# Kernel optimization log

Measured on AMD Instinct MI355X. Metric: run time of the kernel, lower is better.

The kernel has to match this reference:

```python
import jax, jax.numpy as jnp
import numpy as np

K = 64        # num_clusters
S1 = 5        # num_shadow + 1
C = 128       # dim
ALPHA = 1500.0
EPS = 1e-12


def setup_inputs() -> dict:
    key = jax.random.key(0)
    k1, k2 = jax.random.split(key)
    x = jax.random.normal(k1, (8, C, 44, 44), dtype=jnp.float32)
    centroids = jax.random.normal(k2, (K, S1, C), dtype=jnp.float32) * 0.01
    return {"x": x, "centroids": centroids}


def reference(x, centroids):
    N = x.shape[0]
    # conv params derived from centroids, as in _init_params
    w = (2.0 * ALPHA) * centroids.reshape(K * S1, C)            # (K*S1, C)
    b = -ALPHA * jnp.linalg.norm(centroids.reshape(K * S1, C), axis=1)  # (K*S1,)

    xf = x.reshape(N, C, -1)                                    # (N, C, P)
    # 1x1 conv == GEMM over channel dim
    logits = jnp.einsum('mc,ncp->nmp', w, xf) + b[None, :, None]
    logits = logits.reshape(N, K, S1, -1)                       # (N, K, S1, P)

    soft_alpha = jax.nn.softmax(logits[:, :, 0:1, :], axis=1)   # (N, K, 1, P)
    soft_beta = jax.nn.softmax(logits, axis=2)[:, :, 0:1, :]    # (N, K, 1, P)
    soft_assign = soft_alpha * soft_beta                        # (N, K, 1, P)

    # residual = x - rep_centroid; then residual *= (1 + soft_assign); sum over P.
    # sum_p (x[n,c,p] - rep[k,c]) * w[n,k,p]
    #   = einsum(w, x) - rep[k,c] * sum_p w[n,k,p]   (same math, no (N,K,C,P) tensor)
    w_assign = 1.0 + soft_assign[:, :, 0, :]                    # (N, K, P)
    rep = centroids[:, 0, :]                                    # (K, C)
    out = jnp.einsum('nkp,ncp->nkc', w_assign, xf) \
          - rep[None, :, :] * jnp.sum(w_assign, axis=-1)[:, :, None]  # (N, K, C)

    # intra-cluster L2 normalize (dim=2), flatten, global L2 normalize
    out = out / jnp.maximum(jnp.linalg.norm(out, axis=2, keepdims=True), EPS)
    flat = out.reshape(N, -1)
    flat = flat / jnp.maximum(jnp.linalg.norm(flat, axis=1, keepdims=True), EPS)
    return (flat, soft_assign)
```

## Files before the change

### kernel.cpp

```cpp
#include <hip/hip_runtime.h>
#include <math.h>

#define NB 8
#define KC 64
#define S1C 5
#define CC 128
#define PP 1936
#define MM 320
#define PT 64
#define NPT 31
#define NTILE (NB * NPT)
#define ALPHAF 1500.0f
#define EPSF 1e-12f

#define WS_PS   ((size_t)NTILE * KC * CC)
#define WS_MAIN_FLOATS (WS_PS + (size_t)NTILE * KC)
#define WS_FB_ZERO_BYTES ((size_t)(NB * KC * CC + NB * KC) * 4)

typedef __attribute__((ext_vector_type(8))) short short8;
typedef __attribute__((ext_vector_type(4))) float f32x4;

__device__ __forceinline__ unsigned pack_bf16s(float x) {
    unsigned u  = __float_as_uint(x);
    unsigned hi = u & 0xffff0000u;
    float lo    = x - __uint_as_float(hi);
    return hi | (__float_as_uint(lo) >> 16);
}

__device__ __forceinline__ void unpack8(const int4 q0, const int4 q1,
                                        short8& h, short8& l) {
    const int d[8] = {q0.x, q0.y, q0.z, q0.w, q1.x, q1.y, q1.z, q1.w};
#pragma unroll
    for (int j = 0; j < 8; ++j) {
        h[j] = (short)((unsigned)d[j] >> 16);
        l[j] = (short)((unsigned)d[j] & 0xffffu);
    }
}

__device__ __forceinline__ void split8(const float4 a, const float4 b,
                                       short8& h, short8& l) {
    const float f[8] = {a.x, a.y, a.z, a.w, b.x, b.y, b.z, b.w};
#pragma unroll
    for (int j = 0; j < 8; ++j) {
        const unsigned u  = __float_as_uint(f[j]);
        const unsigned hi = u & 0xffff0000u;
        const float lo    = f[j] - __uint_as_float(hi);
        h[j] = (short)(hi >> 16);
        l[j] = (short)(__float_as_uint(lo) >> 16);
    }
}

__global__ __launch_bounds__(1024, 4) void k1_main(
    const float* __restrict__ x, const float* __restrict__ cen,
    float* __restrict__ sa_out, float* __restrict__ outC,
    float* __restrict__ outS, int mode)
{
    __shared__ unsigned xbuf[CC * 68];
    __shared__ unsigned war[KC * 68];
    __shared__ float2   ap[16 * 66];
    __shared__ float    bias_p[512];

    const int tid  = threadIdx.x;
    const int lane = tid & 63;
    const int wid  = tid >> 6;
    const int quad = lane >> 4;
    const int l15  = lane & 15;
    const int bx   = blockIdx.x;
    const int n    = bx / NPT;
    const int pt   = bx - n * NPT;
    const int p0   = pt * PT;

    const float* xn = x + (size_t)n * CC * PP;
    for (int idx = tid; idx < CC * 16; idx += 1024) {
        const int c = idx >> 4;
        const int q = idx & 15;
        const int p = 4 * q;
        float4 v = make_float4(0.f, 0.f, 0.f, 0.f);
        if (p0 + p < PP) v = *(const float4*)(xn + (size_t)c * PP + p0 + p);
        xbuf[(p + 0) * 132 + c] = pack_bf16s(v.x);
        xbuf[(p + 1) * 132 + c] = pack_bf16s(v.y);
        xbuf[(p + 2) * 132 + c] = pack_bf16s(v.z);
        xbuf[(p + 3) * 132 + c] = pack_bf16s(v.w);
    }
    if (tid < 192) bias_p[8 * (tid / 3) + 5 + (tid % 3)] = -3.0e38f;
    if (tid < MM) {
        const float4* row = (const float4*)(cen + (size_t)tid * CC);
        float ss = 0.f;
#pragma unroll
        for (int c4 = 0; c4 < 32; ++c4) {
            const float4 v = row[c4];
            ss += v.x * v.x + v.y * v.y + v.z * v.z + v.w * v.w;
        }
        bias_p[8 * (tid / 5) + (tid % 5)] = -ALPHAF * sqrtf(ss);
    }
    __syncthreads();

    f32x4 dacc[4][2];
#pragma unroll
    for (int a = 0; a < 4; ++a) {
        dacc[a][0] = (f32x4){0.f, 0.f, 0.f, 0.f};
        dacc[a][1] = (f32x4){0.f, 0.f, 0.f, 0.f};
    }
    int mp[2], wrow[2]; bool wvalid[2];
#pragma unroll
    for (int i = 0; i < 2; ++i) {
        mp[i] = (2 * wid + i) * 16 + l15;
        const int s = mp[i] & 7;
        wvalid[i] = (s < 5);
        wrow[i] = 5 * (mp[i] >> 3) + s;
    }

#pragma unroll 1
    for (int ks = 0; ks < 4; ++ks) {
        short8 bh[2], bl[2];
#pragma unroll
        for (int i = 0; i < 2; ++i) {
            float4 wlo = make_float4(0.f, 0.f, 0.f, 0.f);
            float4 whi = make_float4(0.f, 0.f, 0.f, 0.f);
            if (wvalid[i]) {
                const float* wp = cen + (size_t)wrow[i] * CC + ks * 32 + quad * 8;
                wlo = *(const float4*)wp;
                whi = *(const float4*)(wp + 4);
            }
            split8(wlo, whi, bh[i], bl[i]);
        }
#pragma unroll
        for (int a = 0; a < 4; ++a) {
            const int abase = (a * 16 + l15) * 132 + ks * 32 + quad * 8;
            const int4 q0 = *(const int4*)(&xbuf[abase]);
            const int4 q1 = *(const int4*)(&xbuf[abase + 4]);
            short8 ah, al;
            unpack8(q0, q1, ah, al);
#pragma unroll
            for (int i = 0; i < 2; ++i) {
                dacc[a][i] = __builtin_amdgcn_mfma_f32_16x16x32_bf16(ah, bh[i], dacc[a][i], 0, 0, 0);
                dacc[a][i] = __builtin_amdgcn_mfma_f32_16x16x32_bf16(ah, bl[i], dacc[a][i], 0, 0, 0);
                dacc[a][i] = __builtin_amdgcn_mfma_f32_16x16x32_bf16(al, bh[i], dacc[a][i], 0, 0, 0);
            }
        }
    }

    const float bv0 = bias_p[mp[0]];
    const float bv1 = bias_p[mp[1]];
#pragma unroll
    for (int a = 0; a < 4; ++a)
#pragma unroll
        for (int r = 0; r < 4; ++r) {
            dacc[a][0][r] = 2.f * ALPHAF * dacc[a][0][r] + bv0;
            dacc[a][1][r] = 2.f * ALPHAF * dacc[a][1][r] + bv1;
        }

#pragma unroll
    for (int a = 0; a < 4; ++a) {
        f32x4 mx4, se4;
#pragma unroll
        for (int r = 0; r < 4; ++r) {
            float m_ = fmaxf(dacc[a][0][r], dacc[a][1][r]);
            m_ = fmaxf(m_, __shfl_xor(m_, 8));
            float se = __expf(dacc[a][0][r] - m_) + __expf(dacc[a][1][r] - m_);
            se += __shfl_xor(se, 8);
            mx4[r] = m_; se4[r] = se;
        }
        if (l15 == 0) {
#pragma unroll
            for (int r = 0; r < 4; ++r)
                ap[wid * 66 + a * 16 + 4 * quad + r] = make_float2(mx4[r], se4[r]);
        }
    }
    __syncthreads();

    float gmv, arv;
    {
        float gm = -3.0e38f;
#pragma unroll
        for (int w = 0; w < 16; ++w) gm = fmaxf(gm, ap[w * 66 + lane].x);
        float s = 0.f;
#pragma unroll
        for (int w = 0; w < 16; ++w) {
            const float2 v = ap[w * 66 + lane];
            s += v.y * __expf(v.x - gm);
        }
        gmv = gm; arv = 1.0f / s;
    }

    float* san = sa_out + (size_t)n * KC * PP;
    float psum[2] = {0.f, 0.f};
    const bool is_s0 = ((l15 & 7) == 0);
#pragma unroll
    for (int a = 0; a < 4; ++a) {
#pragma unroll
        for (int i = 0; i < 2; ++i) {
            const f32x4 lg = dacc[a][i];
            f32x4 sav; unsigned wpk[4];
#pragma unroll
            for (int r = 0; r < 4; ++r) {
                float m_ = lg[r];
                m_ = fmaxf(m_, __shfl_xor(m_, 1));
                m_ = fmaxf(m_, __shfl_xor(m_, 2));
                m_ = fmaxf(m_, __shfl_xor(m_, 4));
                const float e_ = __expf(lg[r] - m_);
                float d_ = e_;
                d_ += __shfl_xor(d_, 1);
                d_ += __shfl_xor(d_, 2);
                d_ += __shfl_xor(d_, 4);
                const int p = a * 16 + 4 * quad + r;
                const float gm_p = __shfl(gmv, p);
                const float ar_p = __shfl(arv, p);
                const float sa = __expf(lg[r] - gm_p) * ar_p * (e_ / d_);
                const bool pvalid = (p0 + p) < PP;
                const float wa = pvalid ? (1.0f + sa) : 0.0f;
                sav[r] = sa;
                wpk[r] = pack_bf16s(wa);
                psum[i] += wa;
            }
            const int k = 4 * wid + 2 * i + (l15 >> 3);
            if (is_s0) {
                *(int4*)(&war[k * 68 + a * 16 + 4 * quad]) = *(const int4*)wpk;
                const int pg = p0 + a * 16 + 4 * quad;
                if (pg < PP) *(float4*)(&san[(size_t)k * PP + pg]) = *(const float4*)&sav;
            }
        }
    }
#pragma unroll
    for (int i = 0; i < 2; ++i) {
        float s = psum[i];
        s += __shfl_xor(s, 16);
        s += __shfl_xor(s, 32);
        if (is_s0 && quad == 0) {
            const int k = 4 * wid + 2 * i + (l15 >> 3);
            if (mode == 0) outS[(size_t)bx * KC + k] = s;
            else           atomicAdd(&outS[(size_t)n * KC + k], s);
        }
    }
    {
        const int c  = tid >> 3;
        const int po = (tid & 7) * 8;
        float4 v0 = make_float4(0.f, 0.f, 0.f, 0.f), v1 = v0;
        if (p0 + po < PP) {
            const float* src = xn + (size_t)c * PP + p0 + po;
            v0 = *(const float4*)src;
            v1 = *(const float4*)(src + 4);
        }
        unsigned pk[8];
        pk[0] = pack_bf16s(v0.x); pk[1] = pack_bf16s(v0.y);
        pk[2] = pack_bf16s(v0.z); pk[3] = pack_bf16s(v0.w);
        pk[4] = pack_bf16s(v1.x); pk[5] = pack_bf16s(v1.y);
        pk[6] = pack_bf16s(v1.z); pk[7] = pack_bf16s(v1.w);
        *(int4*)(&xbuf[c * 68 + po])     = *(const int4*)&pk[0];
        *(int4*)(&xbuf[c * 68 + po + 4]) = *(const int4*)&pk[4];
    }
    __syncthreads();

    const int kt  = wid & 3;
    const int ct0 = (wid >> 2) * 2;
    f32x4 cacc[2];
    cacc[0] = (f32x4){0.f, 0.f, 0.f, 0.f};
    cacc[1] = (f32x4){0.f, 0.f, 0.f, 0.f};
#pragma unroll
    for (int ks = 0; ks < 64; ks += 32) {
        const int abase = (kt * 16 + l15) * 68 + ks + quad * 8;
        const int4 qa0 = *(const int4*)(&war[abase]);
        const int4 qa1 = *(const int4*)(&war[abase + 4]);
        short8 ah, al;
        unpack8(qa0, qa1, ah, al);
#pragma unroll
        for (int t = 0; t < 2; ++t) {
            const int c = (ct0 + t) * 16 + l15;
            const int bbase = c * 68 + ks + quad * 8;
            const int4 qb0 = *(const int4*)(&xbuf[bbase]);
            const int4 qb1 = *(const int4*)(&xbuf[bbase + 4]);
            short8 bh, bl;
            unpack8(qb0, qb1, bh, bl);
            cacc[t] = __builtin_amdgcn_mfma_f32_16x16x32_bf16(ah, bh, cacc[t], 0, 0, 0);
            cacc[t] = __builtin_amdgcn_mfma_f32_16x16x32_bf16(ah, bl, cacc[t], 0, 0, 0);
            cacc[t] = __builtin_amdgcn_mfma_f32_16x16x32_bf16(al, bh, cacc[t], 0, 0, 0);
        }
    }
    if (mode == 0) {
        float* dst = outC + (size_t)bx * KC * CC;
#pragma unroll
        for (int t = 0; t < 2; ++t) {
            const int c = (ct0 + t) * 16 + l15;
#pragma unroll
            for (int r = 0; r < 4; ++r)
                dst[(kt * 16 + 4 * quad + r) * CC + c] = cacc[t][r];
        }
    } else {
        float* dst = outC + (size_t)n * KC * CC;
#pragma unroll
        for (int t = 0; t < 2; ++t) {
            const int c = (ct0 + t) * 16 + l15;
#pragma unroll
            for (int r = 0; r < 4; ++r)
                atomicAdd(&dst[(kt * 16 + 4 * quad + r) * CC + c], cacc[t][r]);
        }
    }
}

__global__ __launch_bounds__(128) void k2_slab(
    const float* __restrict__ part, const float* __restrict__ ps,
    const float* __restrict__ cen, float* __restrict__ flat)
{
    __shared__ float w2[2];
    const int b = blockIdx.x;
    const int n = b >> 6;
    const int k = b & 63;
    const int c = threadIdx.x;
    const float* pb = part + (size_t)n * NPT * KC * CC + (size_t)k * CC + c;
    float v = 0.f;
#pragma unroll 8
    for (int pt = 0; pt < NPT; ++pt) v += pb[(size_t)pt * KC * CC];
    const float* psb = ps + (size_t)n * NPT * KC + k;
    float sw = 0.f;
#pragma unroll
    for (int pt = 0; pt < NPT; ++pt) sw += psb[(size_t)pt * KC];
    v -= cen[(size_t)k * S1C * CC + c] * sw;

    float ss = v * v;
#pragma unroll
    for (int off = 32; off > 0; off >>= 1) ss += __shfl_down(ss, off);
    if ((c & 63) == 0) w2[c >> 6] = ss;
    __syncthreads();
    const float norm = sqrtf(w2[0] + w2[1]);
    const float scale = 1.0f / (fmaxf(norm, EPSF) * 8.0f);
    flat[(size_t)b * CC + c] = v * scale;
}

__global__ __launch_bounds__(128) void k2_final(
    const float* __restrict__ accC, const float* __restrict__ accS,
    const float* __restrict__ cen, float* __restrict__ flat)
{
    __shared__ float w2[2];
    const int b = blockIdx.x;
    const int k = b & 63;
    const int c = threadIdx.x;
    const float v = accC[(size_t)b * CC + c] -
                    cen[(size_t)k * S1C * CC + c] * accS[b];
    float ss = v * v;
#pragma unroll
    for (int off = 32; off > 0; off >>= 1) ss += __shfl_down(ss, off);
    if ((c & 63) == 0) w2[c >> 6] = ss;
    __syncthreads();
    const float norm = sqrtf(w2[0] + w2[1]);
    const float scale = 1.0f / (fmaxf(norm, EPSF) * 8.0f);
    flat[(size_t)b * CC + c] = v * scale;
}

extern "C" void kernel_launch(void* const* d_in, const int* in_sizes, int n_in,
                              void* d_out, int out_size, void* d_ws, size_t ws_size,
                              hipStream_t stream) {
    const float* x   = (const float*)d_in[0];
    const float* cen = (const float*)d_in[1];
    float* out  = (float*)d_out;
    float* flat = out;
    float* sa   = out + (size_t)NB * KC * CC;
    float* ws   = (float*)d_ws;

    if (ws_size >= WS_MAIN_FLOATS * 4) {
        float* part = ws;
        float* ps   = ws + WS_PS;
        k1_main<<<NTILE, 1024, 0, stream>>>(x, cen, sa, part, ps, 0);
        k2_slab<<<NB * KC, 128, 0, stream>>>(part, ps, cen, flat);
    } else {
        float* accC = ws;
        float* accS = ws + NB * KC * CC;
        hipMemsetAsync(d_ws, 0, WS_FB_ZERO_BYTES, stream);
        k1_main<<<NTILE, 1024, 0, stream>>>(x, cen, sa, accC, accS, 1);
        k2_final<<<NB * KC, 128, 0, stream>>>(accC, accS, cen, flat);
    }
}
```

Baseline: 94.29 us.

## Halve pixel tile to 32 and restructure main kernel for 512 threads

Shrinks the per-block pixel tile from 64 to 32, which doubles the grid to 488 blocks of 512 threads. The aim is to fill more compute units than the old 248-block grid did. X is now staged in LDS as separate hi/lo bf16 arrays, and the second GEMM reads and splits x directly from global memory instead of repacking it into LDS. The slab reduction kernel now reduces the per-tile weight sums in parallel. In exchange the per-tile partial workspace doubles in size, adding global write and read traffic, and each block gets less reuse per byte loaded.

```diff
diff --git a/kernel.cpp b/kernel.cpp
--- a/kernel.cpp
+++ b/kernel.cpp
@@ -7,14 +7,14 @@
 #define CC 128
 #define PP 1936
 #define MM 320
-#define PT 64
-#define NPT 31
+#define PT 32
+#define NPT 61
 #define NTILE (NB * NPT)
 #define ALPHAF 1500.0f
 #define EPSF 1e-12f
 
 #define WS_PS   ((size_t)NTILE * KC * CC)
-#define WS_MAIN_FLOATS (WS_PS + (size_t)NTILE * KC)
+#define WS_MAIN_BYTES ((WS_PS + (size_t)NTILE * KC) * 4)
 #define WS_FB_ZERO_BYTES ((size_t)(NB * KC * CC + NB * KC) * 4)
 
 typedef __attribute__((ext_vector_type(8))) short short8;
@@ -26,7 +26,6 @@
     float lo    = x - __uint_as_float(hi);
     return hi | (__float_as_uint(lo) >> 16);
 }
-
 __device__ __forceinline__ void unpack8(const int4 q0, const int4 q1,
                                         short8& h, short8& l) {
     const int d[8] = {q0.x, q0.y, q0.z, q0.w, q1.x, q1.y, q1.z, q1.w};
@@ -36,7 +35,6 @@
         l[j] = (short)((unsigned)d[j] & 0xffffu);
     }
 }
-
 __device__ __forceinline__ void split8(const float4 a, const float4 b,
                                        short8& h, short8& l) {
     const float f[8] = {a.x, a.y, a.z, a.w, b.x, b.y, b.z, b.w};
@@ -50,15 +48,16 @@
     }
 }
 
-__global__ __launch_bounds__(1024, 4) void k1_main(
+__global__ __launch_bounds__(512, 4) void k1_main(
     const float* __restrict__ x, const float* __restrict__ cen,
     float* __restrict__ sa_out, float* __restrict__ outC,
     float* __restrict__ outS, int mode)
 {
-    __shared__ unsigned xbuf[CC * 68];
-    __shared__ unsigned war[KC * 68];
-    __shared__ float2   ap[16 * 66];
-    __shared__ float    bias_p[512];
+    __shared__ unsigned short xh[PT * 136];
+    __shared__ unsigned short xl[PT * 136];
+    __shared__ unsigned war[KC * 36];
+    __shared__ float2 ap[8 * 33];
+    __shared__ float bias_p[512];
 
     const int tid  = threadIdx.x;
     const int lane = tid & 63;
@@ -71,216 +70,193 @@
     const int p0   = pt * PT;
 
     const float* xn = x + (size_t)n * CC * PP;
-    for (int idx = tid; idx < CC * 16; idx += 1024) {
-        const int c = idx >> 4;
-        const int q = idx & 15;
-        const int p = 4 * q;
+#pragma unroll
+    for (int r = 0; r < 2; ++r) {
+        const int idx = tid + 512 * r;
+        const int c  = idx >> 3;
+        const int qp = idx & 7;
         float4 v = make_float4(0.f, 0.f, 0.f, 0.f);
-        if (p0 + p < PP) v = *(const float4*)(xn + (size_t)c * PP + p0 + p);
-        xbuf[(p + 0) * 132 + c] = pack_bf16s(v.x);
-        xbuf[(p + 1) * 132 + c] = pack_bf16s(v.y);
-        xbuf[(p + 2) * 132 + c] = pack_bf16s(v.z);
-        xbuf[(p + 3) * 132 + c] = pack_bf16s(v.w);
-    }
-    if (tid < 192) bias_p[8 * (tid / 3) + 5 + (tid % 3)] = -3.0e38f;
-    if (tid < MM) {
-        const float4* row = (const float4*)(cen + (size_t)tid * CC);
-        float ss = 0.f;
-#pragma unroll
-        for (int c4 = 0; c4 < 32; ++c4) {
-            const float4 v = row[c4];
-            ss += v.x * v.x + v.y * v.y + v.z * v.z + v.w * v.w;
-        }
-        bias_p[8 * (tid / 5) + (tid % 5)] = -ALPHAF * sqrtf(ss);
-    }
-    __syncthreads();
-
-    f32x4 dacc[4][2];
-#pragma unroll
-    for (int a = 0; a < 4; ++a) {
-        dacc[a][0] = (f32x4){0.f, 0.f, 0.f, 0.f};
-        dacc[a][1] = (f32x4){0.f, 0.f, 0.f, 0.f};
-    }
-    int mp[2], wrow[2]; bool wvalid[2];
-#pragma unroll
-    for (int i = 0; i < 2; ++i) {
-        mp[i] = (2 * wid + i) * 16 + l15;
+        if (p0 + 4 * qp + 3 < PP) v = *(const float4*)(xn + (size_t)c * PP + p0 + 4 * qp);
+        const float f[4] = {v.x, v.y, v.z, v.w};
+#pragma unroll
+        for (int j = 0; j < 4; ++j) {
+            const unsigned u = pack_bf16s(f[j]);
+            const int p = 4 * qp + j;
+            xh[p * 136 + c] = (unsigned short)(u >> 16);
+            xl[p * 136 + c] = (unsigned short)(u & 0xffffu);
+        }
+    }
+    {
+        const int s = tid & 7;
+        if (s < 5) {
+            const float4* row = (const float4*)(cen + (size_t)(5 * (tid >> 3) + s) * CC);
+            float ss = 0.f;
+#pragma unroll
+            for (int c4 = 0; c4 < 32; ++c4) {
+                const float4 v = row[c4];
+                ss += v.x * v.x + v.y * v.y + v.z * v.z + v.w * v.w;
+            }
+            bias_p[tid] = -ALPHAF * sqrtf(ss);
+        } else {
+            bias_p[tid] = -3.0e38f;
+        }
+    }
+    __syncthreads();
+
+    int mp[4]; bool wv[4]; const float* wptr[4];
+#pragma unroll
+    for (int i = 0; i < 4; ++i) {
+        mp[i] = (4 * wid + i) * 16 + l15;
         const int s = mp[i] & 7;
-        wvalid[i] = (s < 5);
-        wrow[i] = 5 * (mp[i] >> 3) + s;
-    }
-
-#pragma unroll 1
+        wv[i]   = (s < 5);
+        wptr[i] = cen + (size_t)(5 * (mp[i] >> 3) + s) * CC;
+    }
+    f32x4 dacc[2][4];
+#pragma unroll
+    for (int a = 0; a < 2; ++a)
+#pragma unroll
+        for (int i = 0; i < 4; ++i) dacc[a][i] = (f32x4){0.f, 0.f, 0.f, 0.f};
+
+#pragma unroll
     for (int ks = 0; ks < 4; ++ks) {
-        short8 bh[2], bl[2];
-#pragma unroll
-        for (int i = 0; i < 2; ++i) {
-            float4 wlo = make_float4(0.f, 0.f, 0.f, 0.f);
-            float4 whi = make_float4(0.f, 0.f, 0.f, 0.f);
-            if (wvalid[i]) {
-                const float* wp = cen + (size_t)wrow[i] * CC + ks * 32 + quad * 8;
-                wlo = *(const float4*)wp;
-                whi = *(const float4*)(wp + 4);
-            }
-            split8(wlo, whi, bh[i], bl[i]);
-        }
-#pragma unroll
-        for (int a = 0; a < 4; ++a) {
-            const int abase = (a * 16 + l15) * 132 + ks * 32 + quad * 8;
-            const int4 q0 = *(const int4*)(&xbuf[abase]);
-            const int4 q1 = *(const int4*)(&xbuf[abase + 4]);
-            short8 ah, al;
-            unpack8(q0, q1, ah, al);
-#pragma unroll
-            for (int i = 0; i < 2; ++i) {
-                dacc[a][i] = __builtin_amdgcn_mfma_f32_16x16x32_bf16(ah, bh[i], dacc[a][i], 0, 0, 0);
-                dacc[a][i] = __builtin_amdgcn_mfma_f32_16x16x32_bf16(ah, bl[i], dacc[a][i], 0, 0, 0);
-                dacc[a][i] = __builtin_amdgcn_mfma_f32_16x16x32_bf16(al, bh[i], dacc[a][i], 0, 0, 0);
-            }
-        }
-    }
-
-    const float bv0 = bias_p[mp[0]];
-    const float bv1 = bias_p[mp[1]];
-#pragma unroll
-    for (int a = 0; a < 4; ++a)
+        short8 ah[2], al[2];
+#pragma unroll
+        for (int a = 0; a < 2; ++a) {
+            const int xo = (a * 16 + l15) * 136 + ks * 32 + quad * 8;
+            ah[a] = *(const short8*)(&xh[xo]);
+            al[a] = *(const short8*)(&xl[xo]);
+        }
+#pragma unroll
+        for (int i = 0; i < 4; ++i) {
+            short8 bh = (short8){0,0,0,0,0,0,0,0};
+            short8 bl = (short8){0,0,0,0,0,0,0,0};
+            if (wv[i]) {
+                const float* wp = wptr[i] + ks * 32 + quad * 8;
+                split8(*(const float4*)wp, *(const float4*)(wp + 4), bh, bl);
+            }
+#pragma unroll
+            for (int a = 0; a < 2; ++a) {
+                dacc[a][i] = __builtin_amdgcn_mfma_f32_16x16x32_bf16(ah[a], bh, dacc[a][i], 0, 0, 0);
+                dacc[a][i] = __builtin_amdgcn_mfma_f32_16x16x32_bf16(ah[a], bl, dacc[a][i], 0, 0, 0);
+                dacc[a][i] = __builtin_amdgcn_mfma_f32_16x16x32_bf16(al[a], bh, dacc[a][i], 0, 0, 0);
+            }
+        }
+    }
+
+    float bv[4];
+#pragma unroll
+    for (int i = 0; i < 4; ++i) bv[i] = bias_p[mp[i]];
+#pragma unroll
+    for (int a = 0; a < 2; ++a) {
+#pragma unroll
+        for (int i = 0; i < 4; ++i)
+#pragma unroll
+            for (int r = 0; r < 4; ++r)
+                dacc[a][i][r] = 2.f * ALPHAF * dacc[a][i][r] + bv[i];
 #pragma unroll
         for (int r = 0; r < 4; ++r) {
-            dacc[a][0][r] = 2.f * ALPHAF * dacc[a][0][r] + bv0;
-            dacc[a][1][r] = 2.f * ALPHAF * dacc[a][1][r] + bv1;
-        }
-
-#pragma unroll
-    for (int a = 0; a < 4; ++a) {
-        f32x4 mx4, se4;
-#pragma unroll
-        for (int r = 0; r < 4; ++r) {
-            float m_ = fmaxf(dacc[a][0][r], dacc[a][1][r]);
+            float m_ = fmaxf(fmaxf(dacc[a][0][r], dacc[a][1][r]),
+                             fmaxf(dacc[a][2][r], dacc[a][3][r]));
             m_ = fmaxf(m_, __shfl_xor(m_, 8));
-            float se = __expf(dacc[a][0][r] - m_) + __expf(dacc[a][1][r] - m_);
+            float se = __expf(dacc[a][0][r] - m_) + __expf(dacc[a][1][r] - m_) +
+                       __expf(dacc[a][2][r] - m_) + __expf(dacc[a][3][r] - m_);
             se += __shfl_xor(se, 8);
-            mx4[r] = m_; se4[r] = se;
-        }
-        if (l15 == 0) {
-#pragma unroll
-            for (int r = 0; r < 4; ++r)
-                ap[wid * 66 + a * 16 + 4 * quad + r] = make_float2(mx4[r], se4[r]);
-        }
-    }
-    __syncthreads();
-
-    float gmv, arv;
-    {
-        float gm = -3.0e38f;
-#pragma unroll
-        for (int w = 0; w < 16; ++w) gm = fmaxf(gm, ap[w * 66 + lane].x);
-        float s = 0.f;
-#pragma unroll
-        for (int w = 0; w < 16; ++w) {
-            const float2 v = ap[w * 66 + lane];
-            s += v.y * __expf(v.x - gm);
-        }
-        gmv = gm; arv = 1.0f / s;
-    }
+            if (l15 == 0) ap[wid * 33 + a * 16 + 4 * quad + r] = make_float2(m_, se);
+        }
+    }
+    __syncthreads();
+
+    const int myp = lane & 31;
+    float2 pv[8];
+#pragma unroll
+    for (int w = 0; w < 8; ++w) pv[w] = ap[w * 33 + myp];
+    float gm = pv[0].x;
+#pragma unroll
+    for (int w = 1; w < 8; ++w) gm = fmaxf(gm, pv[w].x);
+    float ssum = 0.f;
+#pragma unroll
+    for (int w = 0; w < 8; ++w) ssum += pv[w].y * __expf(pv[w].x - gm);
+    const float arcs = 1.0f / ssum;
 
     float* san = sa_out + (size_t)n * KC * PP;
-    float psum[2] = {0.f, 0.f};
-    const bool is_s0 = ((l15 & 7) == 0);
-#pragma unroll
-    for (int a = 0; a < 4; ++a) {
-#pragma unroll
-        for (int i = 0; i < 2; ++i) {
-            const f32x4 lg = dacc[a][i];
-            f32x4 sav; unsigned wpk[4];
+    const bool s0 = ((l15 & 7) == 0);
+#pragma unroll
+    for (int i = 0; i < 4; ++i) {
+        const int k = 8 * wid + 2 * i + (l15 >> 3);
+        float psum = 0.f;
+#pragma unroll
+        for (int a = 0; a < 2; ++a) {
+            const int pg = p0 + a * 16 + 4 * quad;
+            const bool pvld = pg < PP;
+            float sav[4]; unsigned wpk[4];
 #pragma unroll
             for (int r = 0; r < 4; ++r) {
-                float m_ = lg[r];
-                m_ = fmaxf(m_, __shfl_xor(m_, 1));
-                m_ = fmaxf(m_, __shfl_xor(m_, 2));
-                m_ = fmaxf(m_, __shfl_xor(m_, 4));
-                const float e_ = __expf(lg[r] - m_);
-                float d_ = e_;
-                d_ += __shfl_xor(d_, 1);
-                d_ += __shfl_xor(d_, 2);
-                d_ += __shfl_xor(d_, 4);
+                const float lg = dacc[a][i][r];
+                float m5 = lg;
+                m5 = fmaxf(m5, __shfl_xor(m5, 1));
+                m5 = fmaxf(m5, __shfl_xor(m5, 2));
+                m5 = fmaxf(m5, __shfl_xor(m5, 4));
+                const float e = __expf(lg - m5);
+                float d = e;
+                d += __shfl_xor(d, 1);
+                d += __shfl_xor(d, 2);
+                d += __shfl_xor(d, 4);
                 const int p = a * 16 + 4 * quad + r;
-                const float gm_p = __shfl(gmv, p);
-                const float ar_p = __shfl(arv, p);
-                const float sa = __expf(lg[r] - gm_p) * ar_p * (e_ / d_);
-                const bool pvalid = (p0 + p) < PP;
-                const float wa = pvalid ? (1.0f + sa) : 0.0f;
+                const float gmp = __shfl(gm, p);
+                const float arp = __shfl(arcs, p);
+                const float sa = __expf(lg - gmp) * arp * (e / d);
+                const float wa = pvld ? (1.0f + sa) : 0.0f;
                 sav[r] = sa;
                 wpk[r] = pack_bf16s(wa);
-                psum[i] += wa;
-            }
-            const int k = 4 * wid + 2 * i + (l15 >> 3);
-            if (is_s0) {
-                *(int4*)(&war[k * 68 + a * 16 + 4 * quad]) = *(const int4*)wpk;
-                const int pg = p0 + a * 16 + 4 * quad;
-                if (pg < PP) *(float4*)(&san[(size_t)k * PP + pg]) = *(const float4*)&sav;
-            }
-        }
-    }
-#pragma unroll
-    for (int i = 0; i < 2; ++i) {
-        float s = psum[i];
-        s += __shfl_xor(s, 16);
-        s += __shfl_xor(s, 32);
-        if (is_s0 && quad == 0) {
-            const int k = 4 * wid + 2 * i + (l15 >> 3);
-            if (mode == 0) outS[(size_t)bx * KC + k] = s;
-            else           atomicAdd(&outS[(size_t)n * KC + k], s);
-        }
-    }
+                psum += wa;
+            }
+            if (s0) {
+                *(int4*)(&war[k * 36 + a * 16 + 4 * quad]) =
+                    make_int4((int)wpk[0], (int)wpk[1], (int)wpk[2], (int)wpk[3]);
+                if (pvld) *(float4*)(&san[(size_t)k * PP + pg]) =
+                    make_float4(sav[0], sav[1], sav[2], sav[3]);
+            }
+        }
+        psum += __shfl_xor(psum, 16);
+        psum += __shfl_xor(psum, 32);
+        if (s0 && quad == 0) {
+            if (mode == 0) outS[(size_t)bx * KC + k] = psum;
+            else           atomicAdd(&outS[(size_t)n * KC + k], psum);
+        }
+    }
+    __syncthreads();
+
+    const int kt = wid & 3;
+    const int cg = wid >> 2;
+    short8 ah2, al2;
     {
-        const int c  = tid >> 3;
-        const int po = (tid & 7) * 8;
-        float4 v0 = make_float4(0.f, 0.f, 0.f, 0.f), v1 = v0;
-        if (p0 + po < PP) {
-            const float* src = xn + (size_t)c * PP + p0 + po;
-            v0 = *(const float4*)src;
-            v1 = *(const float4*)(src + 4);
-        }
-        unsigned pk[8];
-        pk[0] = pack_bf16s(v0.x); pk[1] = pack_bf16s(v0.y);
-        pk[2] = pack_bf16s(v0.z); pk[3] = pack_bf16s(v0.w);
-        pk[4] = pack_bf16s(v1.x); pk[5] = pack_bf16s(v1.y);
-        pk[6] = pack_bf16s(v1.z); pk[7] = pack_bf16s(v1.w);
-        *(int4*)(&xbuf[c * 68 + po])     = *(const int4*)&pk[0];
-        *(int4*)(&xbuf[c * 68 + po + 4]) = *(const int4*)&pk[4];
-    }
-    __syncthreads();
-
-    const int kt  = wid & 3;
-    const int ct0 = (wid >> 2) * 2;
-    f32x4 cacc[2];
-    cacc[0] = (f32x4){0.f, 0.f, 0.f, 0.f};
-    cacc[1] = (f32x4){0.f, 0.f, 0.f, 0.f};
-#pragma unroll
-    for (int ks = 0; ks < 64; ks += 32) {
-        const int abase = (kt * 16 + l15) * 68 + ks + quad * 8;
-        const int4 qa0 = *(const int4*)(&war[abase]);
-        const int4 qa1 = *(const int4*)(&war[abase + 4]);
-        short8 ah, al;
-        unpack8(qa0, qa1, ah, al);
-#pragma unroll
-        for (int t = 0; t < 2; ++t) {
-            const int c = (ct0 + t) * 16 + l15;
-            const int bbase = c * 68 + ks + quad * 8;
-            const int4 qb0 = *(const int4*)(&xbuf[bbase]);
-            const int4 qb1 = *(const int4*)(&xbuf[bbase + 4]);
-            short8 bh, bl;
-            unpack8(qb0, qb1, bh, bl);
-            cacc[t] = __builtin_amdgcn_mfma_f32_16x16x32_bf16(ah, bh, cacc[t], 0, 0, 0);
-            cacc[t] = __builtin_amdgcn_mfma_f32_16x16x32_bf16(ah, bl, cacc[t], 0, 0, 0);
-            cacc[t] = __builtin_amdgcn_mfma_f32_16x16x32_bf16(al, bh, cacc[t], 0, 0, 0);
-        }
+        const int ao = (kt * 16 + l15) * 36 + quad * 8;
+        const int4 q0 = *(const int4*)(&war[ao]);
+        const int4 q1 = *(const int4*)(&war[ao + 4]);
+        unpack8(q0, q1, ah2, al2);
+    }
+    f32x4 cacc[4];
+#pragma unroll
+    for (int t = 0; t < 4; ++t) cacc[t] = (f32x4){0.f, 0.f, 0.f, 0.f};
+    const int pq = p0 + quad * 8;
+#pragma unroll
+    for (int t = 0; t < 4; ++t) {
+        const int c = (cg * 4 + t) * 16 + l15;
+        short8 bh = (short8){0,0,0,0,0,0,0,0};
+        short8 bl = (short8){0,0,0,0,0,0,0,0};
+        if (pq + 8 <= PP) {
+            const float* src = xn + (size_t)c * PP + pq;
+            split8(*(const float4*)src, *(const float4*)(src + 4), bh, bl);
+        }
+        cacc[t] = __builtin_amdgcn_mfma_f32_16x16x32_bf16(ah2, bh, cacc[t], 0, 0, 0);
+        cacc[t] = __builtin_amdgcn_mfma_f32_16x16x32_bf16(ah2, bl, cacc[t], 0, 0, 0);
+        cacc[t] = __builtin_amdgcn_mfma_f32_16x16x32_bf16(al2, bh, cacc[t], 0, 0, 0);
     }
     if (mode == 0) {
         float* dst = outC + (size_t)bx * KC * CC;
 #pragma unroll
-        for (int t = 0; t < 2; ++t) {
-            const int c = (ct0 + t) * 16 + l15;
+        for (int t = 0; t < 4; ++t) {
+            const int c = (cg * 4 + t) * 16 + l15;
 #pragma unroll
             for (int r = 0; r < 4; ++r)
                 dst[(kt * 16 + 4 * quad + r) * CC + c] = cacc[t][r];
@@ -288,8 +264,8 @@
     } else {
         float* dst = outC + (size_t)n * KC * CC;
 #pragma unroll
-        for (int t = 0; t < 2; ++t) {
-            const int c = (ct0 + t) * 16 + l15;
+        for (int t = 0; t < 4; ++t) {
+            const int c = (cg * 4 + t) * 16 + l15;
 #pragma unroll
             for (int r = 0; r < 4; ++r)
                 atomicAdd(&dst[(kt * 16 + 4 * quad + r) * CC + c], cacc[t][r]);
@@ -301,27 +277,33 @@
     const float* __restrict__ part, const float* __restrict__ ps,
     const float* __restrict__ cen, float* __restrict__ flat)
 {
-    __shared__ float w2[2];
+    __shared__ float redA[2];
+    __shared__ float redB[2];
     const int b = blockIdx.x;
     const int n = b >> 6;
     const int k = b & 63;
     const int c = threadIdx.x;
+
+    float pvv = 0.f;
+    if (c < NPT) pvv = ps[((size_t)n * NPT + c) * KC + k];
+#pragma unroll
+    for (int off = 32; off > 0; off >>= 1) pvv += __shfl_down(pvv, off);
+    if ((c & 63) == 0) redA[c >> 6] = pvv;
+    __syncthreads();
+    const float sw = redA[0] + redA[1];
+
     const float* pb = part + (size_t)n * NPT * KC * CC + (size_t)k * CC + c;
     float v = 0.f;
 #pragma unroll 8
     for (int pt = 0; pt < NPT; ++pt) v += pb[(size_t)pt * KC * CC];
-    const float* psb = ps + (size_t)n * NPT * KC + k;
-    float sw = 0.f;
-#pragma unroll
-    for (int pt = 0; pt < NPT; ++pt) sw += psb[(size_t)pt * KC];
     v -= cen[(size_t)k * S1C * CC + c] * sw;
 
     float ss = v * v;
 #pragma unroll
     for (int off = 32; off > 0; off >>= 1) ss += __shfl_down(ss, off);
-    if ((c & 63) == 0) w2[c >> 6] = ss;
-    __syncthreads();
-    const float norm = sqrtf(w2[0] + w2[1]);
+    if ((c & 63) == 0) redB[c >> 6] = ss;
+    __syncthreads();
+    const float norm = sqrtf(redB[0] + redB[1]);
     const float scale = 1.0f / (fmaxf(norm, EPSF) * 8.0f);
     flat[(size_t)b * CC + c] = v * scale;
 }
@@ -356,16 +338,16 @@
     float* sa   = out + (size_t)NB * KC * CC;
     float* ws   = (float*)d_ws;
 
-    if (ws_size >= WS_MAIN_FLOATS * 4) {
+    if (ws_size >= WS_MAIN_BYTES) {
         float* part = ws;
         float* ps   = ws + WS_PS;
-        k1_main<<<NTILE, 1024, 0, stream>>>(x, cen, sa, part, ps, 0);
+        k1_main<<<NTILE, 512, 0, stream>>>(x, cen, sa, part, ps, 0);
         k2_slab<<<NB * KC, 128, 0, stream>>>(part, ps, cen, flat);
     } else {
         float* accC = ws;
         float* accS = ws + NB * KC * CC;
-        hipMemsetAsync(d_ws, 0, WS_FB_ZERO_BYTES, stream);
-        k1_main<<<NTILE, 1024, 0, stream>>>(x, cen, sa, accC, accS, 1);
+        hipMemsetAsync(ws, 0, WS_FB_ZERO_BYTES, stream);
+        k1_main<<<NTILE, 512, 0, stream>>>(x, cen, sa, accC, accS, 1);
         k2_final<<<NB * KC, 128, 0, stream>>>(accC, accS, cen, flat);
     }
 }
```

After: 105.6 us. 12.0% more time.
